# Performance work log

Hardware: AMD Instinct MI355X
Metric: run time of the kernel (lower is better)

## Reference

```python
import jax, jax.numpy as jnp
import numpy as np

DIM = 1024
NUM_HEADS = 16
HEAD_DIM = DIM // NUM_HEADS
SCALE = HEAD_DIM ** (-0.5)


def alibi_slopes(num_heads):
    x = (2 ** 8) ** (1.0 / num_heads)
    return jnp.array([1.0 / x ** (i + 1) for i in range(num_heads)], dtype=jnp.float32)


def setup_inputs() -> dict:
    key = jax.random.key(0)
    ks = jax.random.split(key, 6)
    B, N = 2, 2048
    x = jax.random.normal(ks[0], (B, N, DIM), dtype=jnp.float32)
    s = DIM ** -0.5
    Wq = jax.random.normal(ks[1], (DIM, DIM), dtype=jnp.float32) * s
    Wk = jax.random.normal(ks[2], (DIM, DIM), dtype=jnp.float32) * s
    Wv = jax.random.normal(ks[3], (DIM, DIM), dtype=jnp.float32) * s
    Wp = jax.random.normal(ks[4], (DIM, DIM), dtype=jnp.float32) * s
    bp = jnp.zeros((DIM,), dtype=jnp.float32)
    return {"x": x, "Wq": Wq, "Wk": Wk, "Wv": Wv, "Wp": Wp, "bp": bp}


def reference(x, Wq, Wk, Wv, Wp, bp):
    B, N, C = x.shape
    H, D = NUM_HEADS, HEAD_DIM
    # Linear layers use torch convention: y = x @ W.T
    q = (x @ Wq.T).reshape(B, N, H, D).transpose(0, 2, 1, 3)  # [B,H,N,D]
    k = (x @ Wk.T).reshape(B, N, H, D).transpose(0, 2, 1, 3)
    v = (x @ Wv.T).reshape(B, N, H, D).transpose(0, 2, 1, 3)
    # ALiBi bias: slopes[h] * (j - i), shape [H,N,N]
    rel = (jnp.arange(N)[None, :] - jnp.arange(N)[:, None]).astype(jnp.float32)
    bias = alibi_slopes(H)[:, None, None] * rel  # [H,N,N]
    # NOTE: original code DIVIDES by scale (= head_dim**-0.5), i.e. multiplies by sqrt(D)
    score = jnp.einsum("bhnd,bhmd->bhnm", q, k) / SCALE + bias[None]
    attn = jax.nn.softmax(score, axis=-1)
    out = jnp.einsum("bhnm,bhmd->bhnd", attn, v)
    out = out.transpose(0, 2, 1, 3).reshape(B, N, C)
    return out @ Wp.T + bp
```

## Files before the change

### kernel.cpp

```cpp
#include <hip/hip_runtime.h>
#include <hip/hip_bf16.h>
#include <cstdint>
#include <cstddef>

#define BB 2
#define NN 2048
#define CC 1024
#define HH 16
#define DD 64
#define MM (BB*NN)

typedef __attribute__((ext_vector_type(8))) _Float16 half8;
typedef __attribute__((ext_vector_type(4))) _Float16 half4;
typedef __attribute__((ext_vector_type(4))) float f32x4;

__device__ __forceinline__ float exp2_fast(float x) {
    float r; asm("v_exp_f32 %0, %1" : "=v"(r) : "v"(x)); return r;
}

__device__ __forceinline__ void gl_lds16(const void* g, void* l) {
    __builtin_amdgcn_global_load_lds(
        (const __attribute__((address_space(1))) unsigned int*)g,
        (__attribute__((address_space(3))) unsigned int*)l, 16, 0, 0);
}

__global__ __launch_bounds__(256) void cvt16(
    const float* __restrict__ in, _Float16* __restrict__ out, int n4) {
    int i = blockIdx.x * 256 + threadIdx.x;
    if (i >= n4) return;
    float4 v = ((const float4*)in)[i];
    half4 h = { (_Float16)v.x, (_Float16)v.y, (_Float16)v.z, (_Float16)v.w };
    ((half4*)out)[i] = h;
}

__global__ __launch_bounds__(256) void cvt16w(
    const float* __restrict__ w0, const float* __restrict__ w1,
    const float* __restrict__ w2, const float* __restrict__ w3,
    _Float16* __restrict__ out, int n4) {
    int s = blockIdx.y;
    const float* in = (s == 0) ? w0 : (s == 1) ? w1 : (s == 2) ? w2 : w3;
    _Float16* dst = out + (size_t)s * n4 * 4;
    int i = blockIdx.x * 256 + threadIdx.x;
    if (i >= n4) return;
    float4 v = ((const float4*)in)[i];
    half4 h = { (_Float16)v.x, (_Float16)v.y, (_Float16)v.z, (_Float16)v.w };
    ((half4*)dst)[i] = h;
}

__global__ __launch_bounds__(256) void gemmQKV(
    const _Float16* __restrict__ A, const _Float16* __restrict__ B,
    _Float16* __restrict__ QH, _Float16* __restrict__ KH,
    _Float16* __restrict__ VT, float qscale) {
    __shared__ _Float16 sA[128 * 64];
    __shared__ _Float16 sB[128 * 64];
    const int K = CC;

    const int t = threadIdx.x;
    const int bm = blockIdx.y, bn = blockIdx.x;
    const int w = t >> 6, lane = t & 63;
    const int wr = (w >> 1) * 64, wc = (w & 1) * 64;
    const int lr = lane & 15, lg = lane >> 4;

    f32x4 acc[4][4];
#pragma unroll
    for (int a = 0; a < 4; ++a)
#pragma unroll
        for (int b2 = 0; b2 < 4; ++b2)
#pragma unroll
            for (int e = 0; e < 4; ++e) acc[a][b2][e] = 0.f;

    for (int kt = 0; kt < K; kt += 64) {
#pragma unroll
        for (int p = 0; p < 4; ++p) {
            int u = p * 256 + t;
            int rowu = u >> 3, su = (u & 7) ^ (rowu & 7);
            gl_lds16(A + (size_t)(bm * 128 + rowu) * K + kt + su * 8, sA + u * 8);
            gl_lds16(B + (size_t)(bn * 128 + rowu) * K + kt + su * 8, sB + u * 8);
        }
        __syncthreads();

#pragma unroll
        for (int c = 0; c < 2; ++c) {
            half8 af[4], bf[4];
#pragma unroll
            for (int f = 0; f < 4; ++f) {
                int ra = wr + f * 16 + lr;
                af[f] = *(const half8*)((const char*)sA + ((ra * 128 + c * 64 + lg * 16) ^ ((ra & 7) << 4)));
                int rb = wc + f * 16 + lr;
                bf[f] = *(const half8*)((const char*)sB + ((rb * 128 + c * 64 + lg * 16) ^ ((rb & 7) << 4)));
            }
#pragma unroll
            for (int fi = 0; fi < 4; ++fi)
#pragma unroll
                for (int fj = 0; fj < 4; ++fj)
                    acc[fi][fj] = __builtin_amdgcn_mfma_f32_16x16x32_f16(af[fi], bf[fj], acc[fi][fj], 0, 0, 0);
        }
        __syncthreads();
    }

#pragma unroll
    for (int fi = 0; fi < 4; ++fi)
#pragma unroll
        for (int fj = 0; fj < 4; ++fj) {
            int col = bn * 128 + wc + fj * 16 + lr;
            int sel = col >> 10, c10 = col & 1023;
            int h2 = c10 >> 6, d2 = c10 & 63;
            int rowb = bm * 128 + wr + fi * 16 + lg * 4;
            int b2 = rowb >> 11, n2 = rowb & (NN - 1);
            if (sel == 0) {
#pragma unroll
                for (int e = 0; e < 4; ++e)
                    QH[((size_t)(b2 * HH + h2) * NN + n2 + e) * DD + d2] =
                        (_Float16)(acc[fi][fj][e] * qscale);
            } else if (sel == 1) {
#pragma unroll
                for (int e = 0; e < 4; ++e)
                    KH[((size_t)(b2 * HH + h2) * NN + n2 + e) * DD + d2] =
                        (_Float16)acc[fi][fj][e];
            } else {
                half4 pk = { (_Float16)acc[fi][fj][0], (_Float16)acc[fi][fj][1],
                             (_Float16)acc[fi][fj][2], (_Float16)acc[fi][fj][3] };
                *(half4*)(VT + ((size_t)(b2 * HH + h2) * DD + d2) * NN + n2) = pk;
            }
        }
}

__global__ __launch_bounds__(256) void gemmPROJ(
    const _Float16* __restrict__ A, const _Float16* __restrict__ B,
    const float* __restrict__ bias, float* __restrict__ Cout, int M, int N, int K) {
    __shared__ _Float16 sA[64 * 64];
    __shared__ _Float16 sB[64 * 64];

    const int t = threadIdx.x;
    const int bm = blockIdx.y, bn = blockIdx.x;
    const int w = t >> 6, lane = t & 63;
    const int wr = (w >> 1) * 32, wc = (w & 1) * 32;
    const int lr = lane & 15, lg = lane >> 4;

    f32x4 acc[2][2];
#pragma unroll
    for (int a = 0; a < 2; ++a)
#pragma unroll
        for (int b2 = 0; b2 < 2; ++b2)
#pragma unroll
            for (int e = 0; e < 4; ++e) acc[a][b2][e] = 0.f;

    for (int kt = 0; kt < K; kt += 64) {
#pragma unroll
        for (int p = 0; p < 2; ++p) {
            int u = p * 256 + t;
            int rowu = u >> 3, su = (u & 7) ^ (rowu & 7);
            gl_lds16(A + (size_t)(bm * 64 + rowu) * K + kt + su * 8, sA + u * 8);
            gl_lds16(B + (size_t)(bn * 64 + rowu) * K + kt + su * 8, sB + u * 8);
        }
        __syncthreads();

#pragma unroll
        for (int c = 0; c < 2; ++c) {
            half8 a0, a1, b0, b1;
            {
                int r0 = wr + lr, r1 = wr + 16 + lr;
                a0 = *(const half8*)((const char*)sA + ((r0 * 128 + c * 64 + lg * 16) ^ ((r0 & 7) << 4)));
                a1 = *(const half8*)((const char*)sA + ((r1 * 128 + c * 64 + lg * 16) ^ ((r1 & 7) << 4)));
                int q0 = wc + lr, q1 = wc + 16 + lr;
                b0 = *(const half8*)((const char*)sB + ((q0 * 128 + c * 64 + lg * 16) ^ ((q0 & 7) << 4)));
                b1 = *(const half8*)((const char*)sB + ((q1 * 128 + c * 64 + lg * 16) ^ ((q1 & 7) << 4)));
            }
            acc[0][0] = __builtin_amdgcn_mfma_f32_16x16x32_f16(a0, b0, acc[0][0], 0, 0, 0);
            acc[0][1] = __builtin_amdgcn_mfma_f32_16x16x32_f16(a0, b1, acc[0][1], 0, 0, 0);
            acc[1][0] = __builtin_amdgcn_mfma_f32_16x16x32_f16(a1, b0, acc[1][0], 0, 0, 0);
            acc[1][1] = __builtin_amdgcn_mfma_f32_16x16x32_f16(a1, b1, acc[1][1], 0, 0, 0);
        }
        __syncthreads();
    }

#pragma unroll
    for (int fi = 0; fi < 2; ++fi)
#pragma unroll
        for (int fj = 0; fj < 2; ++fj)
#pragma unroll
            for (int e = 0; e < 4; ++e) {
                int row = bm * 64 + wr + fi * 16 + lg * 4 + e;
                int col = bn * 64 + wc + fj * 16 + lr;
                Cout[(size_t)row * N + col] = acc[fi][fj][e] + bias[col];
            }
}

__global__ __launch_bounds__(256) void attn16(
    const _Float16* __restrict__ Qh, const _Float16* __restrict__ Kh,
    const _Float16* __restrict__ Vt, _Float16* __restrict__ AO) {
    __shared__ _Float16 sK[2][64 * 64];
    __shared__ _Float16 sV[2][64 * 64];
    __shared__ _Float16 sP[4][32 * 64];

    const int t = threadIdx.x, w = t >> 6, lane = t & 63;
    const int lr = lane & 15, lg = lane >> 4;
    const int qb = blockIdx.x, bh = blockIdx.y;
    const int b = bh >> 4, h = bh & 15;
    const int i0 = qb * 128;
    const size_t baseND = (size_t)bh * NN * DD;
    const size_t baseDN = (size_t)bh * DD * NN;

    half8 qf[2][2];
#pragma unroll
    for (int u = 0; u < 2; ++u) {
        const size_t qoff = baseND + (size_t)(i0 + w * 32 + u * 16 + lr) * DD;
        qf[u][0] = *(const half8*)(Qh + qoff + 0 * 32 + lg * 8);
        qf[u][1] = *(const half8*)(Qh + qoff + 1 * 32 + lg * 8);
    }

    f32x4 accO[2][4];
    float m_run[2], l_run[2];
#pragma unroll
    for (int u = 0; u < 2; ++u) {
        m_run[u] = -INFINITY; l_run[u] = 0.f;
#pragma unroll
        for (int c2 = 0; c2 < 4; ++c2)
            accO[u][c2][0] = accO[u][c2][1] = accO[u][c2][2] = accO[u][c2][3] = 0.f;
    }

    const float slope2 = exp2f(-0.5f * (float)(h + 1)) * 1.44269504f;
    const float s64 = slope2 * 64.f;
    f32x4 cini[4];
#pragma unroll
    for (int ct = 0; ct < 4; ++ct)
#pragma unroll
        for (int e = 0; e < 4; ++e)
            cini[ct][e] = slope2 * (float)(ct * 16 + lg * 4 + e);

    auto stage = [&](int buf, int jt) {
#pragma unroll
        for (int p = 0; p < 2; ++p) {
            int u = p * 256 + t;
            int rowu = u >> 3, su = (u & 7) ^ (rowu & 7);
            gl_lds16(Kh + baseND + (size_t)(jt * 64 + rowu) * DD + su * 8, &sK[buf][u * 8]);
            gl_lds16(Vt + baseDN + (size_t)rowu * NN + jt * 64 + su * 8, &sV[buf][u * 8]);
        }
    };

    stage(0, 0);
    __syncthreads();
    int cur = 0;
    float tb = 0.f;

    for (int jt = 0; jt < NN / 64; ++jt) {
        if (jt + 1 < NN / 64) stage(cur ^ 1, jt + 1);

        f32x4 s[2][4];
#pragma unroll
        for (int u = 0; u < 2; ++u)
#pragma unroll
            for (int ct = 0; ct < 4; ++ct) s[u][ct] = cini[ct];

        __builtin_amdgcn_s_setprio(1);
#pragma unroll
        for (int ct = 0; ct < 4; ++ct)
#pragma unroll
            for (int c = 0; c < 2; ++c) {
                int row = ct * 16 + lr;
                half8 kf = *(const half8*)((const char*)&sK[cur][0] +
                    ((row * 128 + c * 64 + lg * 16) ^ ((row & 7) << 4)));
                s[0][ct] = __builtin_amdgcn_mfma_f32_16x16x32_f16(kf, qf[0][c], s[0][ct], 0, 0, 0);
                s[1][ct] = __builtin_amdgcn_mfma_f32_16x16x32_f16(kf, qf[1][c], s[1][ct], 0, 0, 0);
            }
        __builtin_amdgcn_s_setprio(0);

#pragma unroll
        for (int u = 0; u < 2; ++u) {
            float x0 = fmaxf(fmaxf(s[u][0][0], s[u][0][1]), fmaxf(s[u][0][2], s[u][0][3]));
            float x1 = fmaxf(fmaxf(s[u][1][0], s[u][1][1]), fmaxf(s[u][1][2], s[u][1][3]));
            float x2 = fmaxf(fmaxf(s[u][2][0], s[u][2][1]), fmaxf(s[u][2][2], s[u][2][3]));
            float x3 = fmaxf(fmaxf(s[u][3][0], s[u][3][1]), fmaxf(s[u][3][2], s[u][3][3]));
            float mx = fmaxf(fmaxf(x0, x1), fmaxf(x2, x3));
            mx = fmaxf(mx, __shfl_xor(mx, 16, 64));
            mx = fmaxf(mx, __shfl_xor(mx, 32, 64));
            float mxt = mx + tb;
            float msh;
            bool defer = __all(mxt <= m_run[u] + 8.f) != 0;
            if (defer) {
                msh = m_run[u] - tb;
            } else {
                float mnew = fmaxf(m_run[u], mxt);
                float al = exp2_fast(m_run[u] - mnew);
                m_run[u] = mnew;
                msh = mnew - tb;
#pragma unroll
                for (int c2 = 0; c2 < 4; ++c2)
#pragma unroll
                    for (int e = 0; e < 4; ++e) accO[u][c2][e] *= al;
                l_run[u] *= al;
            }
#pragma unroll
            for (int ct = 0; ct < 4; ++ct)
#pragma unroll
                for (int e = 0; e < 4; ++e) s[u][ct][e] = exp2_fast(s[u][ct][e] - msh);
            float y0 = (s[u][0][0] + s[u][0][1]) + (s[u][0][2] + s[u][0][3]);
            float y1 = (s[u][1][0] + s[u][1][1]) + (s[u][1][2] + s[u][1][3]);
            float y2 = (s[u][2][0] + s[u][2][1]) + (s[u][2][2] + s[u][2][3]);
            float y3 = (s[u][3][0] + s[u][3][1]) + (s[u][3][2] + s[u][3][3]);
            float sum = (y0 + y1) + (y2 + y3);
            sum += __shfl_xor(sum, 16, 64);
            sum += __shfl_xor(sum, 32, 64);
            l_run[u] += sum;

#pragma unroll
            for (int ct = 0; ct < 4; ++ct) {
                half4 pk = { (_Float16)s[u][ct][0], (_Float16)s[u][ct][1],
                             (_Float16)s[u][ct][2], (_Float16)s[u][ct][3] };
                int row = u * 16 + lr;
                *(half4*)((char*)sP[w] + ((row * 128 + ct * 32 + lg * 8) ^ ((lr & 7) << 4))) = pk;
            }
        }

        half8 pb[2][2];
#pragma unroll
        for (int u = 0; u < 2; ++u)
#pragma unroll
            for (int c = 0; c < 2; ++c) {
                int row = u * 16 + lr;
                pb[u][c] = *(const half8*)((const char*)sP[w] +
                    ((row * 128 + c * 64 + lg * 16) ^ ((lr & 7) << 4)));
            }
        __builtin_amdgcn_s_setprio(1);
#pragma unroll
        for (int ctd = 0; ctd < 4; ++ctd)
#pragma unroll
            for (int c = 0; c < 2; ++c) {
                int row = ctd * 16 + lr;
                half8 vf = *(const half8*)((const char*)&sV[cur][0] +
                    ((row * 128 + c * 64 + lg * 16) ^ ((row & 7) << 4)));
                accO[0][ctd] = __builtin_amdgcn_mfma_f32_16x16x32_f16(vf, pb[0][c], accO[0][ctd], 0, 0, 0);
                accO[1][ctd] = __builtin_amdgcn_mfma_f32_16x16x32_f16(vf, pb[1][c], accO[1][ctd], 0, 0, 0);
            }
        __builtin_amdgcn_s_setprio(0);

        __syncthreads();
        cur ^= 1;
        tb += s64;
    }

#pragma unroll
    for (int u = 0; u < 2; ++u) {
        float rl = 1.0f / l_run[u];
        const size_t obase = ((size_t)b * NN + i0 + w * 32 + u * 16 + lr) * CC + h * DD;
#pragma unroll
        for (int ctd = 0; ctd < 4; ++ctd) {
            half4 ov = { (_Float16)(accO[u][ctd][0] * rl), (_Float16)(accO[u][ctd][1] * rl),
                         (_Float16)(accO[u][ctd][2] * rl), (_Float16)(accO[u][ctd][3] * rl) };
            *(half4*)(AO + obase + ctd * 16 + lg * 4) = ov;
        }
    }
}

extern "C" void kernel_launch(void* const* d_in, const int* in_sizes, int n_in,
                              void* d_out, int out_size, void* d_ws, size_t ws_size,
                              hipStream_t stream) {
    const float* x  = (const float*)d_in[0];
    const float* Wq = (const float*)d_in[1];
    const float* Wk = (const float*)d_in[2];
    const float* Wv = (const float*)d_in[3];
    const float* Wp = (const float*)d_in[4];
    const float* bp = (const float*)d_in[5];
    float* out = (float*)d_out;

    char* ws = (char*)d_ws;
    const size_t MB = 1024 * 1024;
    _Float16* X16 = (_Float16*)(ws + 0 * MB);
    _Float16* W16 = (_Float16*)(ws + 8 * MB);
    _Float16* QH  = (_Float16*)(ws + 16 * MB);
    _Float16* KH  = (_Float16*)(ws + 24 * MB);
    _Float16* VT  = (_Float16*)(ws + 32 * MB);
    _Float16* AO  = (_Float16*)(ws + 40 * MB);
    _Float16* WP16 = W16 + 3 * 1024 * 1024;

    cvt16<<<4096, 256, 0, stream>>>(x, X16, (MM * CC) / 4);
    cvt16w<<<dim3(1024, 4), 256, 0, stream>>>(Wq, Wk, Wv, Wp, W16, (CC * CC) / 4);

    const float QSCALE = 8.0f * 1.44269504f;
    gemmQKV<<<dim3(3 * CC / 128, MM / 128), 256, 0, stream>>>(X16, W16, QH, KH, VT, QSCALE);

    attn16<<<dim3(NN / 128, BB * HH), 256, 0, stream>>>(QH, KH, VT, AO);

    gemmPROJ<<<dim3(CC / 64, MM / 64), 256, 0, stream>>>(AO, WP16, bp, out, MM, CC, CC);
}
```

Measured before the change: 152.8 us.

## Merge conversion kernels, halve attention query tile, enlarge projection GEMM tile

Fuses the input and weight fp16 conversion kernels into one launch. Shrinks the attention query block from 128 to 64 rows (16 rows per wave), which doubles the grid to 1024 blocks for more occupancy but doubles K/V reloads per query. Grows the projection GEMM tile to 128x64 for more reuse per block, at the cost of fewer blocks. These are three separate tuning ideas spread across the pipeline.

```diff
diff --git a/kernel.cpp b/kernel.cpp
--- a/kernel.cpp
+++ b/kernel.cpp
@@ -24,27 +24,29 @@
         (__attribute__((address_space(3))) unsigned int*)l, 16, 0, 0);
 }
 
-__global__ __launch_bounds__(256) void cvt16(
-    const float* __restrict__ in, _Float16* __restrict__ out, int n4) {
+__global__ __launch_bounds__(256) void cvtAll(
+    const float* __restrict__ x, const float* __restrict__ wq,
+    const float* __restrict__ wk, const float* __restrict__ wv,
+    const float* __restrict__ wp, _Float16* __restrict__ X16,
+    _Float16* __restrict__ W16) {
+    const int NX4 = MM * CC / 4;
+    const int NW4 = CC * CC / 4;
     int i = blockIdx.x * 256 + threadIdx.x;
-    if (i >= n4) return;
-    float4 v = ((const float4*)in)[i];
+    const float4* src;
+    half4* dst;
+    if (i < NX4) {
+        src = (const float4*)x + i;
+        dst = (half4*)X16 + i;
+    } else {
+        int j = i - NX4;
+        int s = j >> 18, off = j & (NW4 - 1);
+        const float* wsel = (s == 0) ? wq : (s == 1) ? wk : (s == 2) ? wv : wp;
+        src = (const float4*)wsel + off;
+        dst = (half4*)(W16 + (size_t)s * CC * CC) + off;
+    }
+    float4 v = *src;
     half4 h = { (_Float16)v.x, (_Float16)v.y, (_Float16)v.z, (_Float16)v.w };
-    ((half4*)out)[i] = h;
-}
-
-__global__ __launch_bounds__(256) void cvt16w(
-    const float* __restrict__ w0, const float* __restrict__ w1,
-    const float* __restrict__ w2, const float* __restrict__ w3,
-    _Float16* __restrict__ out, int n4) {
-    int s = blockIdx.y;
-    const float* in = (s == 0) ? w0 : (s == 1) ? w1 : (s == 2) ? w2 : w3;
-    _Float16* dst = out + (size_t)s * n4 * 4;
-    int i = blockIdx.x * 256 + threadIdx.x;
-    if (i >= n4) return;
-    float4 v = ((const float4*)in)[i];
-    half4 h = { (_Float16)v.x, (_Float16)v.y, (_Float16)v.z, (_Float16)v.w };
-    ((half4*)dst)[i] = h;
+    *dst = h;
 }
 
 __global__ __launch_bounds__(256) void gemmQKV(
@@ -127,60 +129,69 @@
 
 __global__ __launch_bounds__(256) void gemmPROJ(
     const _Float16* __restrict__ A, const _Float16* __restrict__ B,
-    const float* __restrict__ bias, float* __restrict__ Cout, int M, int N, int K) {
-    __shared__ _Float16 sA[64 * 64];
+    const float* __restrict__ bias, float* __restrict__ Cout) {
+    __shared__ _Float16 sA[128 * 64];
     __shared__ _Float16 sB[64 * 64];
+    const int K = CC, N = CC;
 
     const int t = threadIdx.x;
     const int bm = blockIdx.y, bn = blockIdx.x;
     const int w = t >> 6, lane = t & 63;
-    const int wr = (w >> 1) * 32, wc = (w & 1) * 32;
+    const int wr = (w >> 1) * 64, wc = (w & 1) * 32;
     const int lr = lane & 15, lg = lane >> 4;
 
-    f32x4 acc[2][2];
-#pragma unroll
-    for (int a = 0; a < 2; ++a)
+    f32x4 acc[4][2];
+#pragma unroll
+    for (int a = 0; a < 4; ++a)
 #pragma unroll
         for (int b2 = 0; b2 < 2; ++b2)
 #pragma unroll
             for (int e = 0; e < 4; ++e) acc[a][b2][e] = 0.f;
 
     for (int kt = 0; kt < K; kt += 64) {
+#pragma unroll
+        for (int p = 0; p < 4; ++p) {
+            int u = p * 256 + t;
+            int rowu = u >> 3, su = (u & 7) ^ (rowu & 7);
+            gl_lds16(A + (size_t)(bm * 128 + rowu) * K + kt + su * 8, sA + u * 8);
+        }
 #pragma unroll
         for (int p = 0; p < 2; ++p) {
             int u = p * 256 + t;
             int rowu = u >> 3, su = (u & 7) ^ (rowu & 7);
-            gl_lds16(A + (size_t)(bm * 64 + rowu) * K + kt + su * 8, sA + u * 8);
             gl_lds16(B + (size_t)(bn * 64 + rowu) * K + kt + su * 8, sB + u * 8);
         }
         __syncthreads();
 
 #pragma unroll
         for (int c = 0; c < 2; ++c) {
-            half8 a0, a1, b0, b1;
-            {
-                int r0 = wr + lr, r1 = wr + 16 + lr;
-                a0 = *(const half8*)((const char*)sA + ((r0 * 128 + c * 64 + lg * 16) ^ ((r0 & 7) << 4)));
-                a1 = *(const half8*)((const char*)sA + ((r1 * 128 + c * 64 + lg * 16) ^ ((r1 & 7) << 4)));
-                int q0 = wc + lr, q1 = wc + 16 + lr;
-                b0 = *(const half8*)((const char*)sB + ((q0 * 128 + c * 64 + lg * 16) ^ ((q0 & 7) << 4)));
-                b1 = *(const half8*)((const char*)sB + ((q1 * 128 + c * 64 + lg * 16) ^ ((q1 & 7) << 4)));
-            }
-            acc[0][0] = __builtin_amdgcn_mfma_f32_16x16x32_f16(a0, b0, acc[0][0], 0, 0, 0);
-            acc[0][1] = __builtin_amdgcn_mfma_f32_16x16x32_f16(a0, b1, acc[0][1], 0, 0, 0);
-            acc[1][0] = __builtin_amdgcn_mfma_f32_16x16x32_f16(a1, b0, acc[1][0], 0, 0, 0);
-            acc[1][1] = __builtin_amdgcn_mfma_f32_16x16x32_f16(a1, b1, acc[1][1], 0, 0, 0);
-        }
-        __syncthreads();
-    }
-
-#pragma unroll
-    for (int fi = 0; fi < 2; ++fi)
+            half8 af[4], bf[2];
+#pragma unroll
+            for (int f = 0; f < 4; ++f) {
+                int ra = wr + f * 16 + lr;
+                af[f] = *(const half8*)((const char*)sA + ((ra * 128 + c * 64 + lg * 16) ^ ((ra & 7) << 4)));
+            }
+#pragma unroll
+            for (int f = 0; f < 2; ++f) {
+                int rb = wc + f * 16 + lr;
+                bf[f] = *(const half8*)((const char*)sB + ((rb * 128 + c * 64 + lg * 16) ^ ((rb & 7) << 4)));
+            }
+#pragma unroll
+            for (int fi = 0; fi < 4; ++fi)
+#pragma unroll
+                for (int fj = 0; fj < 2; ++fj)
+                    acc[fi][fj] = __builtin_amdgcn_mfma_f32_16x16x32_f16(af[fi], bf[fj], acc[fi][fj], 0, 0, 0);
+        }
+        __syncthreads();
+    }
+
+#pragma unroll
+    for (int fi = 0; fi < 4; ++fi)
 #pragma unroll
         for (int fj = 0; fj < 2; ++fj)
 #pragma unroll
             for (int e = 0; e < 4; ++e) {
-                int row = bm * 64 + wr + fi * 16 + lg * 4 + e;
+                int row = bm * 128 + wr + fi * 16 + lg * 4 + e;
                 int col = bn * 64 + wc + fj * 16 + lr;
                 Cout[(size_t)row * N + col] = acc[fi][fj][e] + bias[col];
             }
@@ -191,33 +202,28 @@
     const _Float16* __restrict__ Vt, _Float16* __restrict__ AO) {
     __shared__ _Float16 sK[2][64 * 64];
     __shared__ _Float16 sV[2][64 * 64];
-    __shared__ _Float16 sP[4][32 * 64];
+    __shared__ _Float16 sP[4][16 * 64];
 
     const int t = threadIdx.x, w = t >> 6, lane = t & 63;
     const int lr = lane & 15, lg = lane >> 4;
     const int qb = blockIdx.x, bh = blockIdx.y;
     const int b = bh >> 4, h = bh & 15;
-    const int i0 = qb * 128;
+    const int i0 = qb * 64;
     const size_t baseND = (size_t)bh * NN * DD;
     const size_t baseDN = (size_t)bh * DD * NN;
 
-    half8 qf[2][2];
-#pragma unroll
-    for (int u = 0; u < 2; ++u) {
-        const size_t qoff = baseND + (size_t)(i0 + w * 32 + u * 16 + lr) * DD;
-        qf[u][0] = *(const half8*)(Qh + qoff + 0 * 32 + lg * 8);
-        qf[u][1] = *(const half8*)(Qh + qoff + 1 * 32 + lg * 8);
-    }
-
-    f32x4 accO[2][4];
-    float m_run[2], l_run[2];
-#pragma unroll
-    for (int u = 0; u < 2; ++u) {
-        m_run[u] = -INFINITY; l_run[u] = 0.f;
-#pragma unroll
-        for (int c2 = 0; c2 < 4; ++c2)
-            accO[u][c2][0] = accO[u][c2][1] = accO[u][c2][2] = accO[u][c2][3] = 0.f;
-    }
+    half8 qf[2];
+    {
+        const size_t qoff = baseND + (size_t)(i0 + w * 16 + lr) * DD;
+        qf[0] = *(const half8*)(Qh + qoff + 0 * 32 + lg * 8);
+        qf[1] = *(const half8*)(Qh + qoff + 1 * 32 + lg * 8);
+    }
+
+    f32x4 accO[4];
+#pragma unroll
+    for (int e = 0; e < 4; ++e)
+        accO[e][0] = accO[e][1] = accO[e][2] = accO[e][3] = 0.f;
+    float m_run = -INFINITY, l_run = 0.f;
 
     const float slope2 = exp2f(-0.5f * (float)(h + 1)) * 1.44269504f;
     const float s64 = slope2 * 64.f;
@@ -246,11 +252,9 @@
     for (int jt = 0; jt < NN / 64; ++jt) {
         if (jt + 1 < NN / 64) stage(cur ^ 1, jt + 1);
 
-        f32x4 s[2][4];
-#pragma unroll
-        for (int u = 0; u < 2; ++u)
-#pragma unroll
-            for (int ct = 0; ct < 4; ++ct) s[u][ct] = cini[ct];
+        f32x4 s[4];
+#pragma unroll
+        for (int ct = 0; ct < 4; ++ct) s[ct] = cini[ct];
 
         __builtin_amdgcn_s_setprio(1);
 #pragma unroll
@@ -260,67 +264,55 @@
                 int row = ct * 16 + lr;
                 half8 kf = *(const half8*)((const char*)&sK[cur][0] +
                     ((row * 128 + c * 64 + lg * 16) ^ ((row & 7) << 4)));
-                s[0][ct] = __builtin_amdgcn_mfma_f32_16x16x32_f16(kf, qf[0][c], s[0][ct], 0, 0, 0);
-                s[1][ct] = __builtin_amdgcn_mfma_f32_16x16x32_f16(kf, qf[1][c], s[1][ct], 0, 0, 0);
+                s[ct] = __builtin_amdgcn_mfma_f32_16x16x32_f16(kf, qf[c], s[ct], 0, 0, 0);
             }
         __builtin_amdgcn_s_setprio(0);
 
-#pragma unroll
-        for (int u = 0; u < 2; ++u) {
-            float x0 = fmaxf(fmaxf(s[u][0][0], s[u][0][1]), fmaxf(s[u][0][2], s[u][0][3]));
-            float x1 = fmaxf(fmaxf(s[u][1][0], s[u][1][1]), fmaxf(s[u][1][2], s[u][1][3]));
-            float x2 = fmaxf(fmaxf(s[u][2][0], s[u][2][1]), fmaxf(s[u][2][2], s[u][2][3]));
-            float x3 = fmaxf(fmaxf(s[u][3][0], s[u][3][1]), fmaxf(s[u][3][2], s[u][3][3]));
-            float mx = fmaxf(fmaxf(x0, x1), fmaxf(x2, x3));
-            mx = fmaxf(mx, __shfl_xor(mx, 16, 64));
-            mx = fmaxf(mx, __shfl_xor(mx, 32, 64));
-            float mxt = mx + tb;
-            float msh;
-            bool defer = __all(mxt <= m_run[u] + 8.f) != 0;
-            if (defer) {
-                msh = m_run[u] - tb;
-            } else {
-                float mnew = fmaxf(m_run[u], mxt);
-                float al = exp2_fast(m_run[u] - mnew);
-                m_run[u] = mnew;
-                msh = mnew - tb;
-#pragma unroll
-                for (int c2 = 0; c2 < 4; ++c2)
-#pragma unroll
-                    for (int e = 0; e < 4; ++e) accO[u][c2][e] *= al;
-                l_run[u] *= al;
-            }
-#pragma unroll
-            for (int ct = 0; ct < 4; ++ct)
-#pragma unroll
-                for (int e = 0; e < 4; ++e) s[u][ct][e] = exp2_fast(s[u][ct][e] - msh);
-            float y0 = (s[u][0][0] + s[u][0][1]) + (s[u][0][2] + s[u][0][3]);
-            float y1 = (s[u][1][0] + s[u][1][1]) + (s[u][1][2] + s[u][1][3]);
-            float y2 = (s[u][2][0] + s[u][2][1]) + (s[u][2][2] + s[u][2][3]);
-            float y3 = (s[u][3][0] + s[u][3][1]) + (s[u][3][2] + s[u][3][3]);
-            float sum = (y0 + y1) + (y2 + y3);
-            sum += __shfl_xor(sum, 16, 64);
-            sum += __shfl_xor(sum, 32, 64);
-            l_run[u] += sum;
-
-#pragma unroll
-            for (int ct = 0; ct < 4; ++ct) {
-                half4 pk = { (_Float16)s[u][ct][0], (_Float16)s[u][ct][1],
-                             (_Float16)s[u][ct][2], (_Float16)s[u][ct][3] };
-                int row = u * 16 + lr;
-                *(half4*)((char*)sP[w] + ((row * 128 + ct * 32 + lg * 8) ^ ((lr & 7) << 4))) = pk;
-            }
-        }
-
-        half8 pb[2][2];
-#pragma unroll
-        for (int u = 0; u < 2; ++u)
-#pragma unroll
-            for (int c = 0; c < 2; ++c) {
-                int row = u * 16 + lr;
-                pb[u][c] = *(const half8*)((const char*)sP[w] +
-                    ((row * 128 + c * 64 + lg * 16) ^ ((lr & 7) << 4)));
-            }
+        float x0 = fmaxf(fmaxf(s[0][0], s[0][1]), fmaxf(s[0][2], s[0][3]));
+        float x1 = fmaxf(fmaxf(s[1][0], s[1][1]), fmaxf(s[1][2], s[1][3]));
+        float x2 = fmaxf(fmaxf(s[2][0], s[2][1]), fmaxf(s[2][2], s[2][3]));
+        float x3 = fmaxf(fmaxf(s[3][0], s[3][1]), fmaxf(s[3][2], s[3][3]));
+        float mx = fmaxf(fmaxf(x0, x1), fmaxf(x2, x3));
+        mx = fmaxf(mx, __shfl_xor(mx, 16, 64));
+        mx = fmaxf(mx, __shfl_xor(mx, 32, 64));
+        float mxt = mx + tb;
+        float msh;
+        bool defer = __all(mxt <= m_run + 8.f) != 0;
+        if (defer) {
+            msh = m_run - tb;
+        } else {
+            float mnew = fmaxf(m_run, mxt);
+            float al = exp2_fast(m_run - mnew);
+            m_run = mnew;
+            msh = mnew - tb;
+#pragma unroll
+            for (int c2 = 0; c2 < 4; ++c2)
+#pragma unroll
+                for (int e = 0; e < 4; ++e) accO[c2][e] *= al;
+            l_run *= al;
+        }
+#pragma unroll
+        for (int ct = 0; ct < 4; ++ct)
+#pragma unroll
+            for (int e = 0; e < 4; ++e) s[ct][e] = exp2_fast(s[ct][e] - msh);
+        float y0 = (s[0][0] + s[0][1]) + (s[0][2] + s[0][3]);
+        float y1 = (s[1][0] + s[1][1]) + (s[1][2] + s[1][3]);
+        float y2 = (s[2][0] + s[2][1]) + (s[2][2] + s[2][3]);
+        float y3 = (s[3][0] + s[3][1]) + (s[3][2] + s[3][3]);
+        float sum = (y0 + y1) + (y2 + y3);
+        sum += __shfl_xor(sum, 16, 64);
+        sum += __shfl_xor(sum, 32, 64);
+        l_run += sum;
+
+#pragma unroll
+        for (int ct = 0; ct < 4; ++ct) {
+            half4 pk = { (_Float16)s[ct][0], (_Float16)s[ct][1],
+                         (_Float16)s[ct][2], (_Float16)s[ct][3] };
+            *(half4*)((char*)sP[w] + ((lr * 128 + ct * 32 + lg * 8) ^ ((lr & 7) << 4))) = pk;
+        }
+
+        half8 pb0 = *(const half8*)((const char*)sP[w] + ((lr * 128 + 0 * 64 + lg * 16) ^ ((lr & 7) << 4)));
+        half8 pb1 = *(const half8*)((const char*)sP[w] + ((lr * 128 + 1 * 64 + lg * 16) ^ ((lr & 7) << 4)));
         __builtin_amdgcn_s_setprio(1);
 #pragma unroll
         for (int ctd = 0; ctd < 4; ++ctd)
@@ -329,8 +321,7 @@
                 int row = ctd * 16 + lr;
                 half8 vf = *(const half8*)((const char*)&sV[cur][0] +
                     ((row * 128 + c * 64 + lg * 16) ^ ((row & 7) << 4)));
-                accO[0][ctd] = __builtin_amdgcn_mfma_f32_16x16x32_f16(vf, pb[0][c], accO[0][ctd], 0, 0, 0);
-                accO[1][ctd] = __builtin_amdgcn_mfma_f32_16x16x32_f16(vf, pb[1][c], accO[1][ctd], 0, 0, 0);
+                accO[ctd] = __builtin_amdgcn_mfma_f32_16x16x32_f16(vf, c ? pb1 : pb0, accO[ctd], 0, 0, 0);
             }
         __builtin_amdgcn_s_setprio(0);
 
@@ -339,16 +330,13 @@
         tb += s64;
     }
 
-#pragma unroll
-    for (int u = 0; u < 2; ++u) {
-        float rl = 1.0f / l_run[u];
-        const size_t obase = ((size_t)b * NN + i0 + w * 32 + u * 16 + lr) * CC + h * DD;
-#pragma unroll
-        for (int ctd = 0; ctd < 4; ++ctd) {
-            half4 ov = { (_Float16)(accO[u][ctd][0] * rl), (_Float16)(accO[u][ctd][1] * rl),
-                         (_Float16)(accO[u][ctd][2] * rl), (_Float16)(accO[u][ctd][3] * rl) };
-            *(half4*)(AO + obase + ctd * 16 + lg * 4) = ov;
-        }
+    float rl = 1.0f / l_run;
+    const size_t obase = ((size_t)b * NN + i0 + w * 16 + lr) * CC + h * DD;
+#pragma unroll
+    for (int ctd = 0; ctd < 4; ++ctd) {
+        half4 ov = { (_Float16)(accO[ctd][0] * rl), (_Float16)(accO[ctd][1] * rl),
+                     (_Float16)(accO[ctd][2] * rl), (_Float16)(accO[ctd][3] * rl) };
+        *(half4*)(AO + obase + ctd * 16 + lg * 4) = ov;
     }
 }
 
@@ -373,13 +361,12 @@
     _Float16* AO  = (_Float16*)(ws + 40 * MB);
     _Float16* WP16 = W16 + 3 * 1024 * 1024;
 
-    cvt16<<<4096, 256, 0, stream>>>(x, X16, (MM * CC) / 4);
-    cvt16w<<<dim3(1024, 4), 256, 0, stream>>>(Wq, Wk, Wv, Wp, W16, (CC * CC) / 4);
+    cvtAll<<<8192, 256, 0, stream>>>(x, Wq, Wk, Wv, Wp, X16, W16);
 
     const float QSCALE = 8.0f * 1.44269504f;
     gemmQKV<<<dim3(3 * CC / 128, MM / 128), 256, 0, stream>>>(X16, W16, QH, KH, VT, QSCALE);
 
-    attn16<<<dim3(NN / 128, BB * HH), 256, 0, stream>>>(QH, KH, VT, AO);
-
-    gemmPROJ<<<dim3(CC / 64, MM / 64), 256, 0, stream>>>(AO, WP16, bp, out, MM, CC, CC);
-}
+    attn16<<<dim3(NN / 64, BB * HH), 256, 0, stream>>>(QH, KH, VT, AO);
+
+    gemmPROJ<<<dim3(CC / 64, MM / 128), 256, 0, stream>>>(AO, WP16, bp, out);
+}
```

After: 162.8 us. +6.6%, slower.
